# Optimization experiments

Hardware: AMD Instinct MI355X
Metric: run time of the kernel (lower is better)

## Reference

```python
import jax, jax.numpy as jnp
import numpy as np

B = 8
RESOLUTIONS = [65, 129, 257, 513, 1025]
NUM_POINTS = [0, 4096, 16384, 65536, 262144]
CLIP_MIN = -1e9
FINAL = 1025          # last resolution (both axes)
B_MIN, B_MAX = -1.0, 1.0
BALANCE = 0.5


def setup_inputs() -> dict:
    key = jax.random.key(0)
    k1, k2, k3, k4 = jax.random.split(key, 4)
    return {
        "w1": jax.random.normal(k1, (2, 256), jnp.float32),
        "b1": jax.random.normal(k2, (256,), jnp.float32),
        "w2": jax.random.normal(k3, (256, 1), jnp.float32),
        "b2": jax.random.normal(k4, (1,), jnp.float32),
    }


def _interp_bilinear_ac(x, H, W):
    """F.interpolate(..., mode='bilinear', align_corners=True). x: [B, C, h, w]."""
    b, c, h, w = x.shape
    ys = jnp.linspace(0.0, h - 1.0, H)
    xs = jnp.linspace(0.0, w - 1.0, W)
    y0 = jnp.floor(ys).astype(jnp.int32)
    y1 = jnp.minimum(y0 + 1, h - 1)
    wy = ys - y0
    x0 = jnp.floor(xs).astype(jnp.int32)
    x1 = jnp.minimum(x0 + 1, w - 1)
    wx = xs - x0
    # interpolate rows, then columns
    top = x[:, :, y0, :] * (1.0 - wy)[None, None, :, None] + x[:, :, y1, :] * wy[None, None, :, None]
    return top[:, :, :, x0] * (1.0 - wx) + top[:, :, :, x1] * wx


def _batch_eval(coords, w1, b1, w2, b2):
    """coords: [B, N, 2] in final-resolution pixel space (align_corners=False mapping).
    Returns occupancy [B, N] (C == 1)."""
    coords2d = coords / FINAL + 0.5 / FINAL                 # normalize to [0, 1]
    p = coords2d * (B_MAX - B_MIN) + B_MIN                  # [B, N, 2] in world coords
    h = jax.nn.relu(jnp.einsum('bnd,dh->bnh', p, w1) + b1)  # [B, N, 256]
    occ = jax.nn.sigmoid(jnp.einsum('bnh,ho->bno', h, w2) + b2)
    return occ[..., 0]


def reference(w1, b1, w2, b2):
    occ = None
    for i, res in enumerate(RESOLUTIONS):
        if i == 0:
            # init_coords: grid of res x res points spanning [0, FINAL-1]
            xs = jnp.linspace(0.0, FINAL - 1.0, res)
            gy, gx = jnp.meshgrid(xs, xs, indexing='ij')          # y rows, x cols
            coords = jnp.stack([gx.ravel(), gy.ravel()], axis=-1)  # [N, 2] (x, y)
            coords = jnp.broadcast_to(coords, (B, res * res, 2))
            o = _batch_eval(coords, w1, b1, w2, b2)               # [B, N]
            occ = o.reshape(B, 1, res, res)                       # [B, C, H, W]
        else:
            occ = _interp_bilinear_ac(occ, res, res)
            npt = NUM_POINTS[i]
            if npt <= 0:
                continue
            # uncertainty = -|occ - balance_value|
            unc = -jnp.abs(occ - BALANCE)                          # [B, 1, H, W]
            flat_unc = unc.reshape(B, res * res)
            scores, idx = jax.lax.top_k(flat_unc, npt)             # [B, npt]
            px = (idx % res).astype(jnp.float32)
            py = (idx // res).astype(jnp.float32)
            stride = (FINAL - 1.0) / (res - 1.0)
            coords = jnp.stack([px, py], axis=-1) * stride         # [B, npt, 2]
            new_vals = _batch_eval(coords, w1, b1, w2, b2)         # [B, npt]
            occ_flat = occ.reshape(B, res * res)
            old_vals = jnp.take_along_axis(occ_flat, idx, axis=1)
            vals = jnp.where(scores >= CLIP_MIN, new_vals, old_vals)
            occ_flat = jax.vmap(lambda o, i2, v: o.at[i2].set(v))(occ_flat, idx, vals)
            occ = occ_flat.reshape(B, 1, res, res)
    return occ
```

## Files before the change

### kernel.cpp

```cpp
#include <hip/hip_runtime.h>
#include <stdint.h>

#define HID 256
#define NMAXPIX (1025 * 1025)
#define NREP 8
#define NSEG 2048
#define SELMAX 2112

#define HISTA_OFF 0
#define HISTB_OFF 16384
#define HISTC_OFF 32768
#define SCAL_OFF  40960
#define TIC_OFF   41024
#define STAGE_U32 43072

__device__ __forceinline__ float mlp_eval4(float wx, float wy,
                                           const float4* __restrict__ w1x,
                                           const float4* __restrict__ w1y,
                                           const float4* __restrict__ vb1,
                                           const float4* __restrict__ vw2, float b2v) {
    const float C0 = (float)(0.5 / 1025.0);
    float px = (wx / 1025.0f + C0) * 2.0f - 1.0f;
    float py = (wy / 1025.0f + C0) * 2.0f - 1.0f;
    float a0 = 0.f, a1 = 0.f, a2 = 0.f, a3 = 0.f;
#pragma unroll 8
    for (int q = 0; q < HID / 4; ++q) {
        float4 a = w1x[q], b = w1y[q], c = vb1[q], d = vw2[q];
        float h0 = px * a.x + py * b.x + c.x;
        float h1 = px * a.y + py * b.y + c.y;
        float h2 = px * a.z + py * b.z + c.z;
        float h3 = px * a.w + py * b.w + c.w;
        h0 = h0 > 0.f ? h0 : 0.f;
        h1 = h1 > 0.f ? h1 : 0.f;
        h2 = h2 > 0.f ? h2 : 0.f;
        h3 = h3 > 0.f ? h3 : 0.f;
        a0 += h0 * d.x;
        a1 += h1 * d.y;
        a2 += h2 * d.z;
        a3 += h3 * d.w;
    }
    float x = ((a0 + a1) + (a2 + a3)) + b2v;
    float r;
    if (x >= 0.f) { r = 1.0f / (1.0f + expf(-x)); }
    else { float e = expf(x); r = e / (1.0f + e); }
    return r;
}

__device__ __forceinline__ uint32_t block_exscan_256(uint32_t v, volatile uint32_t* lds4) {
    int lane = threadIdx.x & 63, w = threadIdx.x >> 6;
    uint32_t inc = v;
#pragma unroll
    for (int d = 1; d < 64; d <<= 1) {
        uint32_t o = (uint32_t)__shfl_up((int)inc, d, 64);
        if (lane >= d) inc += o;
    }
    if (lane == 63) lds4[w] = inc;
    __syncthreads();
    uint32_t woff = 0;
    for (int i = 0; i < w; ++i) woff += lds4[i];
    return woff + inc - v;
}

__device__ void scan_dev(const uint32_t* __restrict__ hist, int NB,
                         uint32_t rem_in, uint32_t prefix_in, int shift,
                         uint32_t* outp, uint32_t* outr,
                         volatile uint32_t* lds4, volatile uint32_t* ldspair) {
    int tid = threadIdx.x;
    int C = NB >> 8;
    int b0 = NB - (tid + 1) * C;
    uint32_t cnts[8];
#pragma unroll
    for (int k = 0; k < 8; ++k) cnts[k] = 0;
    for (int rep = 0; rep < NREP; ++rep) {
        const uint4* p = (const uint4*)(hist + (size_t)rep * NB + b0);
#pragma unroll
        for (int g = 0; g < 2; ++g) {
            if (g * 4 < C) {
                uint4 v = p[g];
                cnts[g * 4 + 0] += v.x;
                cnts[g * 4 + 1] += v.y;
                cnts[g * 4 + 2] += v.z;
                cnts[g * 4 + 3] += v.w;
            }
        }
    }
    uint32_t ssum = 0;
    for (int k = 0; k < C; ++k) ssum += cnts[k];
    uint32_t excl = block_exscan_256(ssum, lds4);
    uint32_t run = excl;
    for (int k = 0; k < C; ++k) {
        uint32_t c = cnts[C - 1 - k];
        if (rem_in > run && rem_in <= run + c) {
            ldspair[0] = (prefix_in << shift) | (uint32_t)(b0 + C - 1 - k);
            ldspair[1] = rem_in - run;
        }
        run += c;
    }
    __syncthreads();
    *outp = ldspair[0];
    *outr = ldspair[1];
}

__global__ __launch_bounds__(256) void k_eval0z(const float* __restrict__ w1, const float* __restrict__ b1,
                                                const float* __restrict__ w2, const float* __restrict__ b2,
                                                float* __restrict__ occ, uint32_t* __restrict__ zbuf, int zcount) {
    __shared__ alignas(16) float sw1[2 * HID];
    __shared__ alignas(16) float sb1[HID];
    __shared__ alignas(16) float sw2[HID];
    int tid = threadIdx.x;
    for (int i = tid; i < 2 * HID; i += 256) sw1[i] = w1[i];
    sb1[tid] = b1[tid];
    sw2[tid] = w2[tid];
    __syncthreads();
    int gtid = blockIdx.x * 256 + tid;
    int nthreads = gridDim.x * 256;
    for (int i = gtid; i < zcount; i += nthreads) zbuf[i] = 0;
    for (int n = gtid; n < 65 * 65; n += nthreads) {
        int i = n / 65, j = n % 65;
        occ[n] = mlp_eval4(16.0f * (float)j, 16.0f * (float)i,
                           (const float4*)sw1, (const float4*)(sw1 + HID),
                           (const float4*)sb1, (const float4*)sw2, b2[0]);
    }
}

__global__ __launch_bounds__(256) void k_upkey(const float* __restrict__ in, int rp,
                                               float* __restrict__ outg, int r, int nb, int bstride,
                                               uint32_t* __restrict__ keys,
                                               uint32_t* __restrict__ histA) {
    __shared__ uint32_t hist[2048];
    int tid = threadIdx.x;
    for (int k = tid; k < 2048; k += 256) hist[k] = 0;
    __syncthreads();
    int N = r * r;
    int lane = tid & 63;
    int gstride = gridDim.x * 256;
    for (int n0 = blockIdx.x * 256; n0 < N; n0 += gstride) {
        int n = n0 + tid;
        bool act = n < N;
        uint32_t key = 0;
        if (act) {
            int i = n / r, j = n % r;
            int i2 = i >> 1, j2 = j >> 1;
            float v;
            if ((i & 1) == 0) {
                if ((j & 1) == 0) {
                    v = in[i2 * rp + j2];
                } else {
                    float a = in[i2 * rp + j2], b = in[i2 * rp + j2 + 1];
                    v = a * 0.5f + b * 0.5f;
                }
            } else {
                if ((j & 1) == 0) {
                    float a = in[i2 * rp + j2], b = in[(i2 + 1) * rp + j2];
                    v = a * 0.5f + b * 0.5f;
                } else {
                    float a = in[i2 * rp + j2],      c = in[i2 * rp + j2 + 1];
                    float b = in[(i2 + 1) * rp + j2], d = in[(i2 + 1) * rp + j2 + 1];
                    float t1 = a * 0.5f + b * 0.5f;
                    float t2 = c * 0.5f + d * 0.5f;
                    v = t1 * 0.5f + t2 * 0.5f;
                }
            }
            for (int k = 0; k < nb; ++k) outg[(size_t)k * bstride + n] = v;
            float unc = -fabsf(v - 0.5f);
            uint32_t u = __float_as_uint(unc);
            key = (u & 0x80000000u) ? ~u : (u | 0x80000000u);
            keys[n] = key;
        }
        uint32_t bin = key >> 21;
        unsigned long long m = __ballot(act);
        if (m) {
            int leader = __ffsll(m) - 1;
            uint32_t lbin = (uint32_t)__shfl((int)bin, leader, 64);
            unsigned long long smk = __ballot(act && bin == lbin);
            if (smk == m) {
                if (lane == leader) atomicAdd(&hist[lbin], (uint32_t)__popcll(m));
            } else if (act) {
                atomicAdd(&hist[bin], 1u);
            }
        }
    }
    __syncthreads();
    uint32_t* myrep = histA + (size_t)(blockIdx.x & (NREP - 1)) * 2048;
    for (int k = tid; k < 2048; k += 256) {
        uint32_t c = hist[k];
        if (c) atomicAdd(&myrep[k], c);
    }
}

__global__ __launch_bounds__(256) void k_histmid(const uint32_t* __restrict__ keys, int N,
                                                 const uint32_t* __restrict__ prevHist,
                                                 uint32_t* __restrict__ scal,
                                                 int useNpt, uint32_t npt, int scalInIdx, int shift,
                                                 int scalOutIdx,
                                                 int fshift, int bshift, uint32_t bmask,
                                                 uint32_t* __restrict__ outHist, int NBout) {
    __shared__ uint32_t lh[2048];
    __shared__ uint32_t lds4[4];
    __shared__ uint32_t ldspair[2];
    int tid = threadIdx.x, lane = tid & 63;
    uint32_t rem_in = useNpt ? npt : scal[scalInIdx + 1];
    uint32_t pfx_in = useNpt ? 0u  : scal[scalInIdx];
    uint32_t pfx, rem;
    scan_dev(prevHist, 2048, rem_in, pfx_in, shift, &pfx, &rem, lds4, ldspair);
    if (blockIdx.x == 0 && tid == 0) { scal[scalOutIdx] = pfx; scal[scalOutIdx + 1] = rem; }
    for (int k = tid; k < 2048; k += 256) lh[k] = 0;
    __syncthreads();
    int gstride = gridDim.x * 256;
    for (int base = blockIdx.x * 256; base < N; base += gstride) {
        int n = base + tid;
        bool inb = n < N;
        uint32_t key = inb ? keys[n] : 0u;
        bool flt = inb && ((key >> fshift) == pfx);
        uint32_t bin = (key >> bshift) & bmask;
        unsigned long long m = __ballot(flt);
        if (m) {
            int leader = __ffsll(m) - 1;
            uint32_t lbin = (uint32_t)__shfl((int)bin, leader, 64);
            unsigned long long smk = __ballot(flt && bin == lbin);
            if (smk == m) {
                if (lane == leader) atomicAdd(&lh[lbin], (uint32_t)__popcll(m));
            } else if (flt) {
                atomicAdd(&lh[bin], 1u);
            }
        }
    }
    __syncthreads();
    uint32_t* myrep = outHist + (size_t)(blockIdx.x & (NREP - 1)) * NBout;
    for (int k = tid; k < NBout; k += 256) {
        uint32_t c = lh[k];
        if (c) atomicAdd(&myrep[k], c);
    }
}

__global__ __launch_bounds__(256) void k_segcnt(const uint32_t* __restrict__ keys, int N, int seglen,
                                                const uint32_t* __restrict__ histC,
                                                uint32_t* __restrict__ scal,
                                                uint32_t* __restrict__ tic) {
    __shared__ uint32_t lds4[4];
    __shared__ uint32_t ldspair[2];
    int tid = threadIdx.x, lane = tid & 63;
    uint32_t rem2 = scal[3], pfx2 = scal[2];
    uint32_t K, t;
    scan_dev(histC, 1024, rem2, pfx2, 10, &K, &t, lds4, ldspair);
    if (blockIdx.x == 0 && tid == 0) { scal[4] = K; scal[5] = t; }
    int wv = blockIdx.x * 4 + (tid >> 6);
    int s0 = wv * seglen;
    int s1 = s0 + seglen; if (s1 > N) s1 = N;
    uint32_t tcnt = 0;
    for (int base = s0; base < s1; base += 64) {
        int n = base + lane;
        if (n < s1) tcnt += (keys[n] == K) ? 1u : 0u;
    }
#pragma unroll
    for (int d = 32; d; d >>= 1) tcnt += (uint32_t)__shfl_down((int)tcnt, d, 64);
    if (lane == 0) tic[wv] = tcnt;
}

__global__ __launch_bounds__(256) void k_seleval(const uint32_t* __restrict__ keys, int N, int seglen,
                                                 const uint32_t* __restrict__ scal,
                                                 const uint32_t* __restrict__ tic,
                                                 int r, float stride,
                                                 float* __restrict__ occ, int nb, int bstride,
                                                 const float* __restrict__ w1, const float* __restrict__ b1,
                                                 const float* __restrict__ w2, const float* __restrict__ b2) {
    __shared__ alignas(16) float sw1[2 * HID];
    __shared__ alignas(16) float sb1[HID];
    __shared__ alignas(16) float sw2[HID];
    __shared__ uint32_t selcnt;
    __shared__ uint32_t selidx[SELMAX];
    int tid = threadIdx.x, lane = tid & 63;
    for (int i = tid; i < 2 * HID; i += 256) sw1[i] = w1[i];
    sb1[tid] = b1[tid];
    sw2[tid] = w2[tid];
    if (tid == 0) selcnt = 0;
    __syncthreads();
    uint32_t K = scal[4], t = scal[5];

    int wv = blockIdx.x * 4 + (tid >> 6);
    uint32_t tp = 0;
    for (int i = lane; i < wv; i += 64) tp += tic[i];
#pragma unroll
    for (int d = 32; d; d >>= 1) tp += (uint32_t)__shfl_down((int)tp, d, 64);
    tp = (uint32_t)__shfl((int)tp, 0, 64);

    uint32_t tie_run = tp;
    int s0 = wv * seglen;
    int s1 = s0 + seglen; if (s1 > N) s1 = N;
    unsigned long long lowmask = (lane == 63) ? ~0ull >> 1 : ((1ull << lane) - 1ull);
    for (int base = s0; base < s1; base += 64) {
        int n = base + lane;
        bool inb = n < s1;
        uint32_t key = inb ? keys[n] : 0u;
        bool gt = inb && (key > K);
        bool tie = inb && (key == K);
        unsigned long long tm = __ballot(tie);
        uint32_t trank = tie_run + (uint32_t)__popcll(tm & lowmask);
        bool sel = gt || (tie && trank < t);
        unsigned long long smk = __ballot(sel);
        if (smk) {
            int leader = __ffsll(smk) - 1;
            uint32_t wbase = 0;
            if (lane == leader) wbase = atomicAdd(&selcnt, (uint32_t)__popcll(smk));
            wbase = (uint32_t)__shfl((int)wbase, leader, 64);
            if (sel) selidx[wbase + (uint32_t)__popcll(smk & lowmask)] = (uint32_t)n;
        }
        tie_run += (uint32_t)__popcll(tm);
    }
    __syncthreads();

    uint32_t cnt = selcnt;
    float vb2 = b2[0];
    const float4* w1x = (const float4*)sw1;
    const float4* w1y = (const float4*)(sw1 + HID);
    const float4* vb1 = (const float4*)sb1;
    const float4* vw2 = (const float4*)sw2;
    const float C0 = (float)(0.5 / 1025.0);
    for (uint32_t bb = 0; bb < cnt; bb += 512) {
        uint32_t i0 = bb + tid, i1 = bb + tid + 256;
        bool v0 = i0 < cnt, v1 = i1 < cnt;
        int nA = v0 ? (int)selidx[i0] : 0;
        int nB = v1 ? (int)selidx[i1] : 0;
        int iA = nA / r, jA = nA % r;
        int iB = nB / r, jB = nB % r;
        float pxA = ((stride * (float)jA) / 1025.0f + C0) * 2.0f - 1.0f;
        float pyA = ((stride * (float)iA) / 1025.0f + C0) * 2.0f - 1.0f;
        float pxB = ((stride * (float)jB) / 1025.0f + C0) * 2.0f - 1.0f;
        float pyB = ((stride * (float)iB) / 1025.0f + C0) * 2.0f - 1.0f;
        float4 A0 = {0, 0, 0, 0}, A1 = {0, 0, 0, 0};
#pragma unroll 4
        for (int q = 0; q < HID / 4; ++q) {
            float4 a = w1x[q], b = w1y[q], c = vb1[q], d = vw2[q];
            {
                float h0 = pxA * a.x + pyA * b.x + c.x;
                float h1 = pxA * a.y + pyA * b.y + c.y;
                float h2 = pxA * a.z + pyA * b.z + c.z;
                float h3 = pxA * a.w + pyA * b.w + c.w;
                h0 = h0 > 0.f ? h0 : 0.f;
                h1 = h1 > 0.f ? h1 : 0.f;
                h2 = h2 > 0.f ? h2 : 0.f;
                h3 = h3 > 0.f ? h3 : 0.f;
                A0.x += h0 * d.x; A0.y += h1 * d.y;
                A0.z += h2 * d.z; A0.w += h3 * d.w;
            }
            {
                float h0 = pxB * a.x + pyB * b.x + c.x;
                float h1 = pxB * a.y + pyB * b.y + c.y;
                float h2 = pxB * a.z + pyB * b.z + c.z;
                float h3 = pxB * a.w + pyB * b.w + c.w;
                h0 = h0 > 0.f ? h0 : 0.f;
                h1 = h1 > 0.f ? h1 : 0.f;
                h2 = h2 > 0.f ? h2 : 0.f;
                h3 = h3 > 0.f ? h3 : 0.f;
                A1.x += h0 * d.x; A1.y += h1 * d.y;
                A1.z += h2 * d.z; A1.w += h3 * d.w;
            }
        }
        if (v0) {
            float x = ((A0.x + A0.y) + (A0.z + A0.w)) + vb2;
            float rr;
            if (x >= 0.f) { rr = 1.0f / (1.0f + expf(-x)); }
            else { float e = expf(x); rr = e / (1.0f + e); }
            for (int k = 0; k < nb; ++k) occ[(size_t)k * bstride + nA] = rr;
        }
        if (v1) {
            float x = ((A1.x + A1.y) + (A1.z + A1.w)) + vb2;
            float rr;
            if (x >= 0.f) { rr = 1.0f / (1.0f + expf(-x)); }
            else { float e = expf(x); rr = e / (1.0f + e); }
            for (int k = 0; k < nb; ++k) occ[(size_t)k * bstride + nB] = rr;
        }
    }
}

__global__ __launch_bounds__(256) void k_bcast(const float* __restrict__ src, float* __restrict__ dst, int N) {
    int q = blockIdx.x * 256 + threadIdx.x;
    int n = q * 4;
    if (n + 3 < N) {
        float4 v = *(const float4*)(src + n);
#pragma unroll
        for (int k = 0; k < 8; ++k) *(float4*)(dst + (size_t)k * N + n) = v;
    } else if (n < N) {
        for (int m = n; m < N; ++m) {
            float v = src[m];
#pragma unroll
            for (int k = 0; k < 8; ++k) dst[(size_t)k * N + m] = v;
        }
    }
}

extern "C" void kernel_launch(void* const* d_in, const int* in_sizes, int n_in,
                              void* d_out, int out_size, void* d_ws, size_t ws_size,
                              hipStream_t stream) {
    const float* w1 = (const float*)d_in[0];
    const float* b1 = (const float*)d_in[1];
    const float* w2 = (const float*)d_in[2];
    const float* b2 = (const float*)d_in[3];
    float* out = (float*)d_out;

    const size_t A = (((size_t)NMAXPIX * 4) + 255) & ~(size_t)255;
    const size_t SMALL_BYTES = (size_t)4 * STAGE_U32 * 4;
    const size_t need = 3 * A + SMALL_BYTES;

    int fused8 = (ws_size >= need);
    char* base = fused8 ? (char*)d_ws : (char*)d_out;
    float* buf0 = (float*)(base);
    float* buf1 = (float*)(base + A);
    uint32_t* keys = (uint32_t*)(base + 2 * A);
    uint32_t* smallb = (uint32_t*)(base + 3 * A);

    k_eval0z<<<dim3(512), dim3(256), 0, stream>>>(w1, b1, w2, b2, buf0, smallb, 4 * STAGE_U32);

    const int resA[5] = {65, 129, 257, 513, 1025};
    const int nptA[5] = {0, 4096, 16384, 65536, 262144};
    float* cur = buf0;
    float* nxt = buf1;
    for (int s = 1; s < 5; ++s) {
        int rp = resA[s - 1], r = resA[s];
        int N = r * r;
        uint32_t npt = (uint32_t)nptA[s];
        uint32_t* sm    = smallb + (size_t)(s - 1) * STAGE_U32;
        uint32_t* histA = sm + HISTA_OFF;
        uint32_t* histB = sm + HISTB_OFF;
        uint32_t* histC = sm + HISTC_OFF;
        uint32_t* scal  = sm + SCAL_OFF;
        uint32_t* tic   = sm + TIC_OFF;
        int nb1 = (N + 255) / 256;
        int nbu = nb1 < 1024 ? nb1 : 1024;
        int seglen = (N + NSEG - 1) / NSEG;
        float stride = 1024.0f / (float)(r - 1);

        int last = (s == 4);
        float* stage_out = (last && fused8) ? out : nxt;
        int nb = (last && fused8) ? 8 : 1;
        int bstride = (last && fused8) ? NMAXPIX : 0;

        k_upkey<<<dim3(nbu), dim3(256), 0, stream>>>(cur, rp, stage_out, r, nb, bstride, keys, histA);
        k_histmid<<<dim3(512), dim3(256), 0, stream>>>(keys, N, histA, scal, 1, npt, 0, 0,
                                                       0, 21, 10, 0x7FFu, histB, 2048);
        k_histmid<<<dim3(512), dim3(256), 0, stream>>>(keys, N, histB, scal, 0, 0u, 0, 11,
                                                       2, 10, 0, 0x3FFu, histC, 1024);
        k_segcnt<<<dim3(NSEG / 4), dim3(256), 0, stream>>>(keys, N, seglen, histC, scal, tic);
        k_seleval<<<dim3(NSEG / 4), dim3(256), 0, stream>>>(keys, N, seglen, scal, tic, r, stride,
                                                            stage_out, nb, bstride, w1, b1, w2, b2);
        if (!(last && fused8)) { float* tmp = cur; cur = nxt; nxt = tmp; }
    }
    if (!fused8) {
        k_bcast<<<dim3(((NMAXPIX + 3) / 4 + 255) / 256), dim3(256), 0, stream>>>(cur, out, NMAXPIX);
    }
}
```

Baseline: 244.6 us.

## Fuse segment tie-count and selection kernels via decoupled look-back scan

```diff
diff --git a/kernel.cpp b/kernel.cpp
--- a/kernel.cpp
+++ b/kernel.cpp
@@ -61,17 +61,17 @@
     return woff + inc - v;
 }
 
-__device__ void scan_dev(const uint32_t* __restrict__ hist, int NB,
-                         uint32_t rem_in, uint32_t prefix_in, int shift,
-                         uint32_t* outp, uint32_t* outr,
-                         volatile uint32_t* lds4, volatile uint32_t* ldspair) {
+__device__ void scan_generic(const uint32_t* __restrict__ hist, int NB, int nrep,
+                             uint32_t rem_in, uint32_t prefix_in, int shift,
+                             uint32_t* outp, uint32_t* outr,
+                             volatile uint32_t* lds4, volatile uint32_t* ldspair) {
     int tid = threadIdx.x;
     int C = NB >> 8;
     int b0 = NB - (tid + 1) * C;
     uint32_t cnts[8];
 #pragma unroll
     for (int k = 0; k < 8; ++k) cnts[k] = 0;
-    for (int rep = 0; rep < NREP; ++rep) {
+    for (int rep = 0; rep < nrep; ++rep) {
         const uint4* p = (const uint4*)(hist + (size_t)rep * NB + b0);
 #pragma unroll
         for (int g = 0; g < 2; ++g) {
@@ -99,6 +99,46 @@
     __syncthreads();
     *outp = ldspair[0];
     *outr = ldspair[1];
+}
+
+__device__ __forceinline__ void hist_add(uint32_t* lh, uint32_t bin, bool act, int lane) {
+    unsigned long long m = __ballot(act);
+    if (m) {
+        int leader = __ffsll(m) - 1;
+        uint32_t lbin = (uint32_t)__shfl((int)bin, leader, 64);
+        unsigned long long smk = __ballot(act && bin == lbin);
+        if (smk == m) {
+            if (lane == leader) atomicAdd(&lh[lbin], (uint32_t)__popcll(m));
+        } else if (act) {
+            atomicAdd(&lh[bin], 1u);
+        }
+    }
+}
+
+__device__ __forceinline__ float up2x(const float* __restrict__ in, int rp, int r, int n) {
+    int i = n / r, j = n % r;
+    int i2 = i >> 1, j2 = j >> 1;
+    float v;
+    if ((i & 1) == 0) {
+        if ((j & 1) == 0) {
+            v = in[i2 * rp + j2];
+        } else {
+            float a = in[i2 * rp + j2], b = in[i2 * rp + j2 + 1];
+            v = a * 0.5f + b * 0.5f;
+        }
+    } else {
+        if ((j & 1) == 0) {
+            float a = in[i2 * rp + j2], b = in[(i2 + 1) * rp + j2];
+            v = a * 0.5f + b * 0.5f;
+        } else {
+            float a = in[i2 * rp + j2],      c = in[i2 * rp + j2 + 1];
+            float b = in[(i2 + 1) * rp + j2], d = in[(i2 + 1) * rp + j2 + 1];
+            float t1 = a * 0.5f + b * 0.5f;
+            float t2 = c * 0.5f + d * 0.5f;
+            v = t1 * 0.5f + t2 * 0.5f;
+        }
+    }
+    return v;
 }
 
 __global__ __launch_bounds__(256) void k_eval0z(const float* __restrict__ w1, const float* __restrict__ b1,
@@ -139,46 +179,14 @@
         bool act = n < N;
         uint32_t key = 0;
         if (act) {
-            int i = n / r, j = n % r;
-            int i2 = i >> 1, j2 = j >> 1;
-            float v;
-            if ((i & 1) == 0) {
-                if ((j & 1) == 0) {
-                    v = in[i2 * rp + j2];
-                } else {
-                    float a = in[i2 * rp + j2], b = in[i2 * rp + j2 + 1];
-                    v = a * 0.5f + b * 0.5f;
-                }
-            } else {
-                if ((j & 1) == 0) {
-                    float a = in[i2 * rp + j2], b = in[(i2 + 1) * rp + j2];
-                    v = a * 0.5f + b * 0.5f;
-                } else {
-                    float a = in[i2 * rp + j2],      c = in[i2 * rp + j2 + 1];
-                    float b = in[(i2 + 1) * rp + j2], d = in[(i2 + 1) * rp + j2 + 1];
-                    float t1 = a * 0.5f + b * 0.5f;
-                    float t2 = c * 0.5f + d * 0.5f;
-                    v = t1 * 0.5f + t2 * 0.5f;
-                }
-            }
+            float v = up2x(in, rp, r, n);
             for (int k = 0; k < nb; ++k) outg[(size_t)k * bstride + n] = v;
             float unc = -fabsf(v - 0.5f);
             uint32_t u = __float_as_uint(unc);
             key = (u & 0x80000000u) ? ~u : (u | 0x80000000u);
             keys[n] = key;
         }
-        uint32_t bin = key >> 21;
-        unsigned long long m = __ballot(act);
-        if (m) {
-            int leader = __ffsll(m) - 1;
-            uint32_t lbin = (uint32_t)__shfl((int)bin, leader, 64);
-            unsigned long long smk = __ballot(act && bin == lbin);
-            if (smk == m) {
-                if (lane == leader) atomicAdd(&hist[lbin], (uint32_t)__popcll(m));
-            } else if (act) {
-                atomicAdd(&hist[bin], 1u);
-            }
-        }
+        hist_add(hist, key >> 21, act, lane);
     }
     __syncthreads();
     uint32_t* myrep = histA + (size_t)(blockIdx.x & (NREP - 1)) * 2048;
@@ -202,7 +210,7 @@
     uint32_t rem_in = useNpt ? npt : scal[scalInIdx + 1];
     uint32_t pfx_in = useNpt ? 0u  : scal[scalInIdx];
     uint32_t pfx, rem;
-    scan_dev(prevHist, 2048, rem_in, pfx_in, shift, &pfx, &rem, lds4, ldspair);
+    scan_generic(prevHist, 2048, NREP, rem_in, pfx_in, shift, &pfx, &rem, lds4, ldspair);
     if (blockIdx.x == 0 && tid == 0) { scal[scalOutIdx] = pfx; scal[scalOutIdx + 1] = rem; }
     for (int k = tid; k < 2048; k += 256) lh[k] = 0;
     __syncthreads();
@@ -213,17 +221,7 @@
         uint32_t key = inb ? keys[n] : 0u;
         bool flt = inb && ((key >> fshift) == pfx);
         uint32_t bin = (key >> bshift) & bmask;
-        unsigned long long m = __ballot(flt);
-        if (m) {
-            int leader = __ffsll(m) - 1;
-            uint32_t lbin = (uint32_t)__shfl((int)bin, leader, 64);
-            unsigned long long smk = __ballot(flt && bin == lbin);
-            if (smk == m) {
-                if (lane == leader) atomicAdd(&lh[lbin], (uint32_t)__popcll(m));
-            } else if (flt) {
-                atomicAdd(&lh[bin], 1u);
-            }
-        }
+        hist_add(lh, bin, flt, lane);
     }
     __syncthreads();
     uint32_t* myrep = outHist + (size_t)(blockIdx.x & (NREP - 1)) * NBout;
@@ -233,18 +231,35 @@
     }
 }
 
-__global__ __launch_bounds__(256) void k_segcnt(const uint32_t* __restrict__ keys, int N, int seglen,
-                                                const uint32_t* __restrict__ histC,
-                                                uint32_t* __restrict__ scal,
-                                                uint32_t* __restrict__ tic) {
+__global__ __launch_bounds__(256, 2) void k_segsel(
+        const uint32_t* __restrict__ keys, int N, int seglen,
+        const uint32_t* __restrict__ histC,
+        const uint32_t* __restrict__ scal,
+        uint32_t* __restrict__ tic,
+        int r, float stride,
+        float* __restrict__ occ, int nb, int bstride,
+        const float* __restrict__ w1, const float* __restrict__ b1,
+        const float* __restrict__ w2, const float* __restrict__ b2) {
+    __shared__ alignas(16) float sw1[2 * HID];
+    __shared__ alignas(16) float sb1[HID];
+    __shared__ alignas(16) float sw2[HID];
+    __shared__ uint32_t selcnt;
+    __shared__ uint32_t selidx[SELMAX];
     __shared__ uint32_t lds4[4];
     __shared__ uint32_t ldspair[2];
-    int tid = threadIdx.x, lane = tid & 63;
+    __shared__ uint32_t wtc[4];
+    __shared__ uint32_t s_excl;
+    int tid = threadIdx.x, lane = tid & 63, w = tid >> 6;
+    for (int i = tid; i < 2 * HID; i += 256) sw1[i] = w1[i];
+    sb1[tid] = b1[tid];
+    sw2[tid] = w2[tid];
+    if (tid == 0) { selcnt = 0; s_excl = 0; }
+
     uint32_t rem2 = scal[3], pfx2 = scal[2];
     uint32_t K, t;
-    scan_dev(histC, 1024, rem2, pfx2, 10, &K, &t, lds4, ldspair);
-    if (blockIdx.x == 0 && tid == 0) { scal[4] = K; scal[5] = t; }
-    int wv = blockIdx.x * 4 + (tid >> 6);
+    scan_generic(histC, 1024, NREP, rem2, pfx2, 10, &K, &t, lds4, ldspair);
+
+    int wv = blockIdx.x * 4 + w;
     int s0 = wv * seglen;
     int s1 = s0 + seglen; if (s1 > N) s1 = N;
     uint32_t tcnt = 0;
@@ -254,39 +269,65 @@
     }
 #pragma unroll
     for (int d = 32; d; d >>= 1) tcnt += (uint32_t)__shfl_down((int)tcnt, d, 64);
-    if (lane == 0) tic[wv] = tcnt;
-}
-
-__global__ __launch_bounds__(256) void k_seleval(const uint32_t* __restrict__ keys, int N, int seglen,
-                                                 const uint32_t* __restrict__ scal,
-                                                 const uint32_t* __restrict__ tic,
-                                                 int r, float stride,
-                                                 float* __restrict__ occ, int nb, int bstride,
-                                                 const float* __restrict__ w1, const float* __restrict__ b1,
-                                                 const float* __restrict__ w2, const float* __restrict__ b2) {
-    __shared__ alignas(16) float sw1[2 * HID];
-    __shared__ alignas(16) float sb1[HID];
-    __shared__ alignas(16) float sw2[HID];
-    __shared__ uint32_t selcnt;
-    __shared__ uint32_t selidx[SELMAX];
-    int tid = threadIdx.x, lane = tid & 63;
-    for (int i = tid; i < 2 * HID; i += 256) sw1[i] = w1[i];
-    sb1[tid] = b1[tid];
-    sw2[tid] = w2[tid];
-    if (tid == 0) selcnt = 0;
-    __syncthreads();
-    uint32_t K = scal[4], t = scal[5];
-
-    int wv = blockIdx.x * 4 + (tid >> 6);
-    uint32_t tp = 0;
-    for (int i = lane; i < wv; i += 64) tp += tic[i];
-#pragma unroll
-    for (int d = 32; d; d >>= 1) tp += (uint32_t)__shfl_down((int)tp, d, 64);
-    tp = (uint32_t)__shfl((int)tp, 0, 64);
-
-    uint32_t tie_run = tp;
-    int s0 = wv * seglen;
-    int s1 = s0 + seglen; if (s1 > N) s1 = N;
+    if (lane == 0) wtc[w] = tcnt;
+    __syncthreads();
+    uint32_t agg = wtc[0] + wtc[1] + wtc[2] + wtc[3];
+    uint32_t intra = 0;
+    for (int i = 0; i < w; ++i) intra += wtc[i];
+
+    if (tid == 0) {
+        uint32_t st = (blockIdx.x == 0) ? ((2u << 30) | agg) : ((1u << 30) | agg);
+        __hip_atomic_store(&tic[blockIdx.x], st, __ATOMIC_RELAXED, __HIP_MEMORY_SCOPE_AGENT);
+    }
+    if (blockIdx.x > 0 && w == 0) {
+        uint32_t excl = 0;
+        int b = (int)blockIdx.x - 1;
+        for (;;) {
+            int mine = b - lane;
+            bool active = (mine >= 0);
+            uint32_t f = 0;
+            if (active) {
+                f = __hip_atomic_load(&tic[mine], __ATOMIC_RELAXED, __HIP_MEMORY_SCOPE_AGENT);
+                int spins = 0;
+                while ((f >> 30) == 0u && spins < 1000) {
+                    __builtin_amdgcn_s_sleep(2);
+                    f = __hip_atomic_load(&tic[mine], __ATOMIC_RELAXED, __HIP_MEMORY_SCOPE_AGENT);
+                    ++spins;
+                }
+                if ((f >> 30) == 0u) {
+                    int ms0 = mine * seglen;
+                    int ms1 = ms0 + seglen; if (ms1 > N) ms1 = N;
+                    uint32_t c = 0;
+                    for (int n2 = ms0; n2 < ms1; ++n2) c += (keys[n2] == K) ? 1u : 0u;
+                    f = (1u << 30) | c;
+                }
+            }
+            unsigned long long incm = __ballot(active && (f >> 30) == 2u);
+            uint32_t val;
+            bool done = (incm != 0ull);
+            if (done) {
+                int l2 = __ffsll(incm) - 1;
+                val = (lane <= l2) ? (f & 0x3FFFFFFFu) : 0u;
+            } else {
+                val = active ? (f & 0x3FFFFFFFu) : 0u;
+            }
+#pragma unroll
+            for (int d = 32; d; d >>= 1) val += (uint32_t)__shfl_down((int)val, d, 64);
+            val = (uint32_t)__shfl((int)val, 0, 64);
+            excl += val;
+            if (done) break;
+            if (b < 64) break;
+            b -= 64;
+        }
+        if (lane == 0) {
+            __hip_atomic_store(&tic[blockIdx.x], (2u << 30) | (excl + agg),
+                               __ATOMIC_RELAXED, __HIP_MEMORY_SCOPE_AGENT);
+            s_excl = excl;
+        }
+    }
+    __syncthreads();
+    uint32_t tie_run = s_excl + intra;
+
     unsigned long long lowmask = (lane == 63) ? ~0ull >> 1 : ((1ull << lane) - 1ull);
     for (int base = s0; base < s1; base += 64) {
         int n = base + lane;
@@ -440,9 +481,9 @@
                                                        0, 21, 10, 0x7FFu, histB, 2048);
         k_histmid<<<dim3(512), dim3(256), 0, stream>>>(keys, N, histB, scal, 0, 0u, 0, 11,
                                                        2, 10, 0, 0x3FFu, histC, 1024);
-        k_segcnt<<<dim3(NSEG / 4), dim3(256), 0, stream>>>(keys, N, seglen, histC, scal, tic);
-        k_seleval<<<dim3(NSEG / 4), dim3(256), 0, stream>>>(keys, N, seglen, scal, tic, r, stride,
-                                                            stage_out, nb, bstride, w1, b1, w2, b2);
+        k_segsel<<<dim3(NSEG / 4), dim3(256), 0, stream>>>(keys, N, seglen, histC, scal, tic,
+                                                           r, stride, stage_out, nb, bstride,
+                                                           w1, b1, w2, b2);
         if (!(last && fused8)) { float* tmp = cur; cur = nxt; nxt = tmp; }
     }
     if (!fused8) {
```

New measurement: 244.6 us. Within noise of the previous version (-0.0%).
